# Kernel optimization log

Measured on AMD Instinct MI355X. Metric: run time of the kernel, lower is better.

The kernel has to match this reference:

```python
import jax, jax.numpy as jnp
import numpy as np

S, B, H, V = 64, 8, 512, 8192  # seq_length, batch, hidden, vocab
NEG = -1e9  # finite stand-in for -inf so gradients stay clean


def setup_inputs() -> dict:
    key = jax.random.key(0)
    ks = jax.random.split(key, 8)
    lin = lambda k, fi, fo: jax.random.normal(k, (fi, fo), jnp.float32) * 0.05
    return dict(
        h=jax.random.normal(ks[0], (S, B, H), jnp.float32) * 0.1,
        sentence=jax.random.randint(ks[1], (S, B), 0, V),
        t_W1=lin(ks[2], 2 * H, H), t_b1=jnp.zeros((H,), jnp.float32),
        t_W2=lin(ks[3], H, 1), t_b2=jnp.zeros((1,), jnp.float32),
        w_W1=lin(ks[4], 2 * H, H), w_b1=jnp.zeros((H,), jnp.float32),
        w_W2=lin(ks[5], H, V), w_b2=jnp.zeros((V,), jnp.float32),
    )


def _inside(h, sentence, t_W1, t_b1, t_W2, t_b2, w_W1, w_b1, w_W2, w_b2):
    sent_length = S - 1
    # ---- transition scores on full (i, j) grid: concat(h_i, h_j) -> MLP -> scalar
    hi = jnp.broadcast_to(h[:, None], (S, S, B, H))
    hj = jnp.broadcast_to(h[None, :], (S, S, B, H))
    feat = jnp.concatenate([hi, hj], axis=-1)                      # [S,S,B,2H]
    t = (jax.nn.relu(feat @ t_W1 + t_b1) @ t_W2 + t_b2)[..., 0]    # [S,S,B]
    sh_lp = jax.nn.log_sigmoid(-t)   # log p(shift | i, j)
    re_lp = jax.nn.log_sigmoid(t)    # log p(reduce | i, j)

    # ---- word generation log-probs for pairs (i, j), i < j <= sent_length-1
    iu, ju = jnp.triu_indices(sent_length, k=1)                    # P pairs
    hp = jnp.concatenate([h[iu], h[ju]], axis=-1)                  # [P,B,2H]
    logits = jax.nn.relu(hp @ w_W1 + w_b1) @ w_W2 + w_b2           # [P,B,V]
    lse = jax.scipy.special.logsumexp(logits, axis=-1)             # [P,B]
    tok = sentence[ju + 1]                                         # [P,B]
    tok_logit = jnp.take_along_axis(logits, tok[..., None], axis=-1)[..., 0]
    word_lp = tok_logit - lse
    # shift prob + word prob (word_prob_list in the original)
    wp = jnp.full((S, S, B), NEG, jnp.float32).at[iu, ju].set(sh_lp[iu, ju] + word_lp)

    # ---- DP table init
    table = jnp.full((S, S, B), NEG, jnp.float32)
    f0 = jnp.concatenate([h[0], h[0]], axis=-1)                    # [B,2H]
    lg0 = jax.nn.relu(f0 @ w_W1 + w_b1) @ w_W2 + w_b2              # [B,V]
    init_lp = jnp.take_along_axis(jax.nn.log_softmax(lg0, axis=-1),
                                  sentence[1][:, None], axis=1)[:, 0]
    table = table.at[0, 1].set(init_lp)
    jd = jnp.arange(1, sent_length)
    table = table.at[jd, jd + 1].set(0.0)

    # ---- diagonal sweep: table[i,j] = LSE_k( table[i,k]+table[k,j]+wp[i,k]+re[k,j] )
    ivec = jnp.arange(S)
    mvec = jnp.arange(1, S)

    def step(tab, g):
        i = ivec[:, None]
        m = mvec[None, :]
        k = jnp.clip(i + m, 0, S - 1)                              # [S,S-1]
        jv = jnp.clip(ivec + g, 0, S - 1)                          # [S]
        j = jv[:, None]
        valid = (m < g) & (ivec[:, None] + g <= sent_length)       # [S,S-1]
        sc = tab[i, k] + tab[k, j] + wp[i, k] + re_lp[k, j]        # [S,S-1,B]
        sc = jnp.where(valid[..., None], sc, NEG)
        mmax = jnp.max(sc, axis=1, keepdims=True)
        new = jnp.log(jnp.sum(jnp.exp(sc - mmax), axis=1)) + mmax[:, 0]
        row_ok = (ivec + g <= sent_length)[:, None]
        tab = tab.at[ivec, jv].set(jnp.where(row_ok, new, tab[ivec, jv]))
        return tab, None

    table, _ = jax.lax.scan(step, table, jnp.arange(2, sent_length + 1))
    final = table[0, sent_length] + re_lp[0, sent_length]          # [B]
    return -jnp.sum(final)  # neg_log_likelihood


def reference(h, sentence, t_W1, t_b1, t_W2, t_b2, w_W1, w_b1, w_W2, w_b2):
    return _inside(h, sentence, t_W1, t_b1, t_W2, t_b2, w_W1, w_b1, w_W2, w_b2)
```

## Files before the change

### kernel.cpp

```cpp
#include <hip/hip_runtime.h>
#include <hip/hip_bf16.h>
#include <hip/hip_fp8.h>
#include <math.h>

#define NEG (-1.0e9f)

typedef __bf16 bf16_t;
typedef __bf16 bf16x4 __attribute__((ext_vector_type(4)));
typedef __bf16 bf16x8 __attribute__((ext_vector_type(8)));
typedef float f32x4 __attribute__((ext_vector_type(4)));
typedef long i64x2 __attribute__((ext_vector_type(2)));
typedef unsigned char u8;
typedef unsigned long long u64;

#define SS 64
#define BB 8
#define HH 512
#define VV 8192
#define NPAIR 1953
#define NPTOT 1954
#define MROWS (NPTOT*BB)
#define MPAD  16384

__device__ __forceinline__ float logsig(float x) {
  return fminf(x, 0.f) - __logf(1.f + __expf(-fabsf(x)));
}
__device__ __forceinline__ u8 f2q(float x) { __hip_fp8_e4m3 q(x); return q.__x; }
__device__ __forceinline__ float q2f(u8 b) { __hip_fp8_e4m3 q; q.__x = b; return (float)q; }
__device__ __forceinline__ int ksl(int c) { return 2 * (c & 3) + (c >> 2); }

__global__ __launch_bounds__(256) void k_prep(
    const float* __restrict__ h,   bf16_t* __restrict__ hbf,
    const float* __restrict__ tW1, bf16_t* __restrict__ tW1T,
    const float* __restrict__ wW1, bf16_t* __restrict__ wW1T) {
  __shared__ float tile[32][33];
  int blk = blockIdx.x, tid = threadIdx.x;
  if (blk < 256) {
    int gi = blk * 256 + tid;
    float4 v = ((const float4*)h)[gi];
    bf16x4 o = {(bf16_t)v.x, (bf16_t)v.y, (bf16_t)v.z, (bf16_t)v.w};
    ((bf16x4*)hbf)[gi] = o;
    return;
  }
  const float* in; bf16_t* out; int R = 1024, C = 512, t;
  if (blk < 768) { in = tW1; out = tW1T; t = blk - 256; }
  else           { in = wW1; out = wW1T; t = blk - 768; }
  int xt = C / 32;
  int c0 = (t % xt) * 32, r0 = (t / xt) * 32;
  int tx = tid & 31, ty = tid >> 5;
  for (int i = ty; i < 32; i += 8)
    tile[i][tx] = in[(size_t)(r0 + i) * C + c0 + tx];
  __syncthreads();
  for (int i = ty; i < 32; i += 8)
    out[(size_t)(c0 + i) * R + r0 + tx] = (bf16_t)tile[tx][i];
}

__global__ __launch_bounds__(256) void k_gemm4t(
    const bf16_t* __restrict__ A,
    const bf16_t* __restrict__ tW1T, const bf16_t* __restrict__ wW1T,
    float* __restrict__ Ut, float* __restrict__ Vt,
    float* __restrict__ Uw, float* __restrict__ Vw,
    const float* __restrict__ wW2, u8* __restrict__ w2t8)
{
  __shared__ __align__(16) char lds_raw[16384];
  const int tid = threadIdx.x;
  if (blockIdx.x >= 64) {
    float* tile = (float*)lds_raw;
    int t = blockIdx.x - 64;
    int c0 = (t % 256) * 32, r0 = (t / 256) * 32;
    int tx = tid & 31, ty = tid >> 5;
    for (int i = ty; i < 32; i += 8)
      tile[i * 33 + tx] = wW2[(size_t)(r0 + i) * 8192 + c0 + tx];
    __syncthreads();
    for (int i = ty; i < 32; i += 8) {
      int k = r0 + tx;
      int pos = (k >> 6) * 64 + ksl((k >> 3) & 7) * 8 + (k & 7);
      w2t8[(size_t)(c0 + i) * 512 + pos] = f2q(tile[tx * 33 + i]);
    }
    return;
  }
  bf16_t* As = (bf16_t*)lds_raw;
  bf16_t* Bs = (bf16_t*)(lds_raw + 8192);
  const int lane = tid & 63;
  const int wave = tid >> 6;
  const int wr = wave >> 1, wc = wave & 1;
  const int sel = blockIdx.x >> 4, sub = blockIdx.x & 15;
  const bf16_t* BT = (sel < 2 ? tW1T : wW1T) + (sel & 1) * 512;
  float* Cout = (sel == 0) ? Ut : (sel == 1) ? Vt : (sel == 2) ? Uw : Vw;
  const int m0 = (sub & 3) * 128, n0 = (sub >> 2) * 128;
  const int lda = 512, ldb = 1024, ldc = 512;

  const int rowS = tid >> 2;
  const int kS = (tid & 3) * 8;
  const bf16_t* gA0 = A + (size_t)(m0 + rowS) * lda + kS;
  const bf16_t* gA1 = A + (size_t)(m0 + rowS + 64) * lda + kS;
  const bf16_t* gB0 = BT + (size_t)(n0 + rowS) * ldb + kS;
  const bf16_t* gB1 = BT + (size_t)(n0 + rowS + 64) * ldb + kS;

  f32x4 acc[4][4] = {};
  const int aoff = (wr * 64 + (lane & 15)) * 32 + (lane >> 4) * 8;
  const int boff = (wc * 64 + (lane & 15)) * 32 + (lane >> 4) * 8;

  for (int k0 = 0; k0 < 512; k0 += 32) {
    __builtin_amdgcn_global_load_lds((const __attribute__((address_space(1))) void*)(gA0 + k0),
        (__attribute__((address_space(3))) void*)(As + wave * 512), 16, 0, 0);
    __builtin_amdgcn_global_load_lds((const __attribute__((address_space(1))) void*)(gA1 + k0),
        (__attribute__((address_space(3))) void*)(As + 2048 + wave * 512), 16, 0, 0);
    __builtin_amdgcn_global_load_lds((const __attribute__((address_space(1))) void*)(gB0 + k0),
        (__attribute__((address_space(3))) void*)(Bs + wave * 512), 16, 0, 0);
    __builtin_amdgcn_global_load_lds((const __attribute__((address_space(1))) void*)(gB1 + k0),
        (__attribute__((address_space(3))) void*)(Bs + 2048 + wave * 512), 16, 0, 0);
    __syncthreads();
    bf16x8 af[4], bfr[4];
    #pragma unroll
    for (int mf = 0; mf < 4; ++mf) af[mf] = *(const bf16x8*)&As[aoff + mf * 16 * 32];
    #pragma unroll
    for (int nf = 0; nf < 4; ++nf) bfr[nf] = *(const bf16x8*)&Bs[boff + nf * 16 * 32];
    #pragma unroll
    for (int mf = 0; mf < 4; ++mf)
      #pragma unroll
      for (int nf = 0; nf < 4; ++nf)
        acc[mf][nf] = __builtin_amdgcn_mfma_f32_16x16x32_bf16(af[mf], bfr[nf], acc[mf][nf], 0, 0, 0);
    __syncthreads();
  }
  #pragma unroll
  for (int mf = 0; mf < 4; ++mf)
    #pragma unroll
    for (int r2 = 0; r2 < 4; ++r2) {
      int grow = m0 + wr * 64 + mf * 16 + (lane >> 4) * 4 + r2;
      #pragma unroll
      for (int nf = 0; nf < 4; ++nf) {
        int gcol = n0 + wc * 64 + nf * 16 + (lane & 15);
        Cout[(size_t)grow * ldc + gcol] = acc[mf][nf][r2];
      }
    }
}

#define STAGEA(b, h, kt) do { \
  const u8* _s = A8 + (size_t)(m0 + (h)*128 + (tid>>2)) * 512 + (kt)*64 + csrc; \
  __builtin_amdgcn_global_load_lds((const __attribute__((address_space(1))) void*)_s, \
    (__attribute__((address_space(3))) void*)(As + (b)*16384 + (h)*8192 + (tid>>6)*1024), 16, 0, 0); \
} while(0)

#define STAGEB(b, h, kt) do { \
  const u8* _s = BT8 + (size_t)(n0 + (h)*128 + (tid>>2)) * 512 + (kt)*64 + csrc; \
  __builtin_amdgcn_global_load_lds((const __attribute__((address_space(1))) void*)_s, \
    (__attribute__((address_space(3))) void*)(Bs + (b)*16384 + (h)*8192 + (tid>>6)*1024), 16, 0, 0); \
} while(0)

#define LDA(b, mh) do { \
  _Pragma("unroll") \
  for (int _m = 0; _m < 4; ++_m) \
    afv[_m] = *(const i64x2*)(As + (b)*16384 + (mh)*8192 + ardE + _m*1024); \
} while(0)

#define LDB(b, nh) do { \
  _Pragma("unroll") \
  for (int _n = 0; _n < 2; ++_n) \
    bfv[nh][_n] = *(const i64x2*)(Bs + (b)*16384 + (nh)*8192 + brdE + _n*1024); \
} while(0)

#define MMA(mh, nh) do { \
  __builtin_amdgcn_s_setprio(1); \
  _Pragma("unroll") \
  for (int _m = 0; _m < 4; ++_m) \
    _Pragma("unroll") \
    for (int _n = 0; _n < 2; ++_n) { \
      acc[(mh)*4+_m][(nh)*2+_n] = __builtin_amdgcn_mfma_f32_16x16x32_fp8_fp8( \
          afv[_m][0], bfv[nh][_n][0], acc[(mh)*4+_m][(nh)*2+_n], 0, 0, 0); \
      acc[(mh)*4+_m][(nh)*2+_n] = __builtin_amdgcn_mfma_f32_16x16x32_fp8_fp8( \
          afv[_m][1], bfv[nh][_n][1], acc[(mh)*4+_m][(nh)*2+_n], 0, 0, 0); \
    } \
  __builtin_amdgcn_s_setprio(0); \
} while(0)

#define BARLG() do { __builtin_amdgcn_s_barrier(); \
  asm volatile("s_waitcnt lgkmcnt(0)" ::: "memory"); \
  __builtin_amdgcn_sched_barrier(0); } while(0)
#define ENDPH() __builtin_amdgcn_s_barrier()
#define CKPT() asm volatile("s_waitcnt vmcnt(2)" ::: "memory")

__global__ __launch_bounds__(512, 2) void k_gemm256(
    const u8* __restrict__ A8,
    const u8* __restrict__ BT8,
    const float* __restrict__ bias,
    float* __restrict__ sumexp)
{
  __shared__ __align__(16) u8 As[2 * 16384];
  __shared__ __align__(16) u8 Bs[2 * 16384];
  const int tid = threadIdx.x;
  const int l = tid & 63;
  const int wave = tid >> 6;
  const int wr = wave >> 2, wc = wave & 3;

  const int xcd = blockIdx.x & 7, sub = blockIdx.x >> 3;
  const int mt = xcd * 8 + (sub & 7);
  const int nt = sub >> 3;
  const int m0 = mt * 256, n0 = nt * 256;

  const int csrc = (((tid & 3) ^ ((tid >> 3) & 3)) << 4);
  const int rsw = (((l >> 4) ^ ((l & 15) >> 1)) & 3) << 4;
  const int ardE = (wr * 64 + (l & 15)) * 64 + rsw;
  const int brdE = (wc * 32 + (l & 15)) * 64 + rsw;

  f32x4 acc[8][4] = {};
  i64x2 afv[4];
  i64x2 bfv[2][2];

  STAGEA(0, 0, 0); STAGEA(0, 1, 0); STAGEB(0, 0, 0); STAGEB(0, 1, 0);
  STAGEA(1, 0, 1); STAGEB(1, 0, 1);
  CKPT();
  __builtin_amdgcn_s_barrier();

  #pragma unroll 1
  for (int t = 0; t < 4; ++t) {
    int tA = 2 * t + 1;
    int tB = 2 * t + 2; if (tB > 7) tB = 7;
    int tC = 2 * t + 3; if (tC > 7) tC = 7;
    LDA(0, 0); LDB(0, 0); LDB(0, 1); STAGEA(1, 1, tA); STAGEB(1, 1, tA);
      BARLG(); MMA(0, 0); MMA(0, 1); ENDPH();
    LDA(0, 1);                       STAGEA(0, 0, tB); STAGEB(0, 0, tB);
      BARLG(); MMA(1, 0); MMA(1, 1); CKPT(); ENDPH();
    LDA(1, 0); LDB(1, 0); LDB(1, 1); STAGEA(0, 1, tB); STAGEB(0, 1, tB);
      BARLG(); MMA(0, 0); MMA(0, 1); ENDPH();
    LDA(1, 1);                       STAGEA(1, 0, tC); STAGEB(1, 0, tC);
      BARLG(); MMA(1, 0); MMA(1, 1); CKPT(); ENDPH();
  }

  float b2v[4];
  #pragma unroll
  for (int nf = 0; nf < 4; ++nf)
    b2v[nf] = bias[n0 + (nf >> 1) * 128 + wc * 32 + (nf & 1) * 16 + (l & 15)];
  #pragma unroll
  for (int mf = 0; mf < 8; ++mf) {
    #pragma unroll
    for (int r2 = 0; r2 < 4; ++r2) {
      float s = 0.f;
      #pragma unroll
      for (int nf = 0; nf < 4; ++nf)
        s += __expf(acc[mf][nf][r2] + b2v[nf]);
      s += __shfl_xor(s, 1); s += __shfl_xor(s, 2);
      s += __shfl_xor(s, 4); s += __shfl_xor(s, 8);
      if ((l & 15) == 0)
        atomicAdd(&sumexp[m0 + (mf >> 2) * 128 + wr * 64 + (mf & 3) * 16 + (l >> 4) * 4 + r2], s);
    }
  }
}

__global__ __launch_bounds__(256) void k_actnet(
    const float* __restrict__ Uw, const float* __restrict__ Vw,
    const float* __restrict__ wb1, u8* __restrict__ act8,
    float* __restrict__ sumexp,
    const u8* __restrict__ w2t8, const int* __restrict__ sent,
    const float* __restrict__ wb2, float* __restrict__ tok_logit,
    const float* __restrict__ Ut, const float* __restrict__ Vt,
    const float* __restrict__ tb1, const float* __restrict__ tW2,
    const float* __restrict__ tb2,
    float* __restrict__ sh_lp, float* __restrict__ re_lp)
{
  __shared__ float ldsf[8192];
  if (blockIdx.x < 2048) {
    float* pd = ldsf;
    int p = blockIdx.x;
    if (threadIdx.x < 8) sumexp[p * 8 + threadIdx.x] = 0.f;
    int iu = 0, ju = 0;
    bool real = (p < NPTOT);
    if (p < NPAIR) {
      int i = 0, base = 0;
      while (base + (62 - i) <= p) { base += 62 - i; ++i; }
      iu = i; ju = i + 1 + (p - base);
    }
    const int srow = (p < NPAIR) ? (ju + 1) : 1;
    for (int t = threadIdx.x; t < 512; t += 256) {
      int b = t >> 6, c = t & 63;
      int wpos = (c >> 3) * 64 + ksl(c & 7) * 8;
      u64 bytes = 0;
      if (real) {
        const float4* u4 = (const float4*)(Uw + (size_t)(iu * BB + b) * HH);
        const float4* v4 = (const float4*)(Vw + (size_t)(ju * BB + b) * HH);
        const float4* bb4 = (const float4*)wb1;
        #pragma unroll
        for (int q = 0; q < 2; ++q) {
          float4 uu = u4[c * 2 + q], vv = v4[c * 2 + q], bb = bb4[c * 2 + q];
          bytes |= (u64)f2q(fmaxf(uu.x + vv.x + bb.x, 0.f)) << (8 * (q * 4 + 0));
          bytes |= (u64)f2q(fmaxf(uu.y + vv.y + bb.y, 0.f)) << (8 * (q * 4 + 1));
          bytes |= (u64)f2q(fmaxf(uu.z + vv.z + bb.z, 0.f)) << (8 * (q * 4 + 2));
          bytes |= (u64)f2q(fmaxf(uu.w + vv.w + bb.w, 0.f)) << (8 * (q * 4 + 3));
        }
      }
      *(u64*)(act8 + (size_t)(p * 8 + b) * 512 + wpos) = bytes;
      float s = 0.f;
      if (real) {
        int tok = sent[srow * BB + b];
        u64 wv = *(const u64*)(w2t8 + (size_t)tok * 512 + wpos);
        #pragma unroll
        for (int e = 0; e < 8; ++e)
          s += q2f((u8)(bytes >> (8 * e))) * q2f((u8)(wv >> (8 * e)));
      }
      pd[t] = s;
    }
    __syncthreads();
    if (real) {
      int wv_ = threadIdx.x >> 6, ln = threadIdx.x & 63;
      #pragma unroll
      for (int rr = 0; rr < 2; ++rr) {
        int b = wv_ * 2 + rr;
        float s = pd[b * 64 + ln];
        #pragma unroll
        for (int off = 1; off < 64; off <<= 1) s += __shfl_xor(s, off);
        if (ln == 0) {
          int tok = sent[srow * BB + b];
          tok_logit[p * 8 + b] = s + wb2[tok];
        }
      }
    }
    return;
  }
  int t = blockIdx.x - 2048;
  int b = t & 7, pr = t >> 3;
  int ig = 0, base = 0;
  while (base + (8 - ig) <= pr) { base += 8 - ig; ++ig; }
  int jg = ig + (pr - base);
  float* Us = ldsf;
  float* Vs = ldsf + 4096;
  for (int q = threadIdx.x; q < 1024; q += 256) {
    int ii = q >> 7, cc = q & 127;
    ((float4*)Us)[ii * 128 + cc] = ((const float4*)(Ut + (size_t)((ig * 8 + ii) * BB + b) * HH))[cc];
    ((float4*)Vs)[ii * 128 + cc] = ((const float4*)(Vt + (size_t)((jg * 8 + ii) * BB + b) * HH))[cc];
  }
  __syncthreads();
  int lane = threadIdx.x & 63, wv_ = threadIdx.x >> 6;
  float b1r[8], w2r[8];
  #pragma unroll
  for (int k = 0; k < 8; ++k) { b1r[k] = tb1[lane + 64 * k]; w2r[k] = tW2[lane + 64 * k]; }
  for (int pp = wv_; pp < 64; pp += 4) {
    int ii = pp >> 3, jj = pp & 7;
    int i = ig * 8 + ii, j = jg * 8 + jj;
    float s = 0.f;
    #pragma unroll
    for (int k = 0; k < 8; ++k)
      s += fmaxf(Us[ii * 512 + lane + 64 * k] + Vs[jj * 512 + lane + 64 * k] + b1r[k], 0.f) * w2r[k];
    #pragma unroll
    for (int off = 1; off < 64; off <<= 1) s += __shfl_xor(s, off);
    if (lane == 0 && i < j) {
      float tv = s + tb2[0];
      re_lp[(i * 64 + j) * 8 + b] = logsig(tv);
      sh_lp[(i * 64 + j) * 8 + b] = logsig(-tv);
    }
  }
}

__global__ __launch_bounds__(1024) void k_dp(const float* __restrict__ sh_lp, const float* __restrict__ re_lp,
                                             const float* __restrict__ tok_logit, const float* __restrict__ sumexp,
                                             float* __restrict__ finals) {
  int b = blockIdx.x;
  __shared__ float tab[4096];
  __shared__ float wpl[4096];
  __shared__ float rel[4096];
  int tid = threadIdx.x;
  for (int idx = tid; idx < 4096; idx += 1024) {
    tab[idx] = NEG;
    int i = idx >> 6, j = idx & 63;
    float w = NEG;
    if (i < j && j <= 62) {
      int p = i * 62 - i * (i - 1) / 2 + (j - i - 1);
      int r = p * 8 + b;
      w = sh_lp[idx * 8 + b] + (tok_logit[r] - __logf(sumexp[r]));
    }
    wpl[idx] = w;
    rel[idx] = (idx >> 6) < (idx & 63) ? re_lp[idx * 8 + b] : NEG;
  }
  __syncthreads();
  if (tid == 0) tab[1] = tok_logit[NPAIR * 8 + b] - __logf(sumexp[NPAIR * 8 + b]);
  if (tid >= 1 && tid <= 62) tab[tid * 64 + tid + 1] = 0.f;
  __syncthreads();
  int lane = tid & 63, wave = tid >> 6;
  for (int g = 2; g <= 63; ++g) {
    int cnt = 64 - g;
    if (g <= 17) {
      int seg = lane >> 4, sl = lane & 15;
      int i = wave * 4 + seg;
      if (i < cnt) {
        int m = sl + 1;
        int j = i + g, k = i + m;
        float sc = NEG;
        if (m < g) sc = tab[i * 64 + k] + tab[k * 64 + j] + wpl[i * 64 + k] + rel[k * 64 + j];
        float mx = sc;
        #pragma unroll
        for (int off = 1; off < 16; off <<= 1) mx = fmaxf(mx, __shfl_xor(mx, off));
        float e = (m < g) ? __expf(sc - mx) : 0.f;
        #pragma unroll
        for (int off = 1; off < 16; off <<= 1) e += __shfl_xor(e, off);
        if (sl == 0) tab[i * 64 + j] = __logf(e) + mx;
      }
    } else {
      for (int i = wave; i < cnt; i += 16) {
        int m = lane + 1;
        int j = i + g, k = i + m;
        float sc = NEG;
        if (m < g) sc = tab[i * 64 + k] + tab[k * 64 + j] + wpl[i * 64 + k] + rel[k * 64 + j];
        float mx = sc;
        #pragma unroll
        for (int off = 1; off < 64; off <<= 1) mx = fmaxf(mx, __shfl_xor(mx, off));
        float e = (m < g) ? __expf(sc - mx) : 0.f;
        #pragma unroll
        for (int off = 1; off < 64; off <<= 1) e += __shfl_xor(e, off);
        if (lane == 0) tab[i * 64 + j] = __logf(e) + mx;
      }
    }
    __syncthreads();
  }
  if (tid == 0) finals[b] = tab[63] + rel[63];
}

__global__ void k_final(const float* __restrict__ finals, float* __restrict__ out) {
  if (threadIdx.x == 0) {
    float s = 0.f;
    for (int b = 0; b < 8; ++b) s += finals[b];
    out[0] = -s;
  }
}

extern "C" void kernel_launch(void* const* d_in, const int* in_sizes, int n_in,
                              void* d_out, int out_size, void* d_ws, size_t ws_size,
                              hipStream_t stream) {
  const float* h    = (const float*)d_in[0];
  const int*   sent = (const int*)d_in[1];
  const float* tW1  = (const float*)d_in[2];
  const float* tb1  = (const float*)d_in[3];
  const float* tW2  = (const float*)d_in[4];
  const float* tb2  = (const float*)d_in[5];
  const float* wW1  = (const float*)d_in[6];
  const float* wb1  = (const float*)d_in[7];
  const float* wW2  = (const float*)d_in[8];
  const float* wb2  = (const float*)d_in[9];
  float* out = (float*)d_out;

  char* ws = (char*)d_ws;
  size_t off = 0;
  auto alloc = [&](size_t bytes) { char* p = ws + off; off += (bytes + 255) & ~(size_t)255; return p; };
  bf16_t* hbf    = (bf16_t*)alloc((size_t)512 * 512 * 2);
  bf16_t* tW1T   = (bf16_t*)alloc((size_t)512 * 1024 * 2);
  bf16_t* wW1T   = (bf16_t*)alloc((size_t)512 * 1024 * 2);
  u8*     w2t8   = (u8*)alloc((size_t)VV * HH);
  float*  Ut     = (float*)alloc((size_t)512 * 512 * 4);
  float*  Vt     = (float*)alloc((size_t)512 * 512 * 4);
  float*  Uw     = (float*)alloc((size_t)512 * 512 * 4);
  float*  Vw     = (float*)alloc((size_t)512 * 512 * 4);
  u8*     act8   = (u8*)alloc((size_t)MPAD * HH);
  float*  sumexp = (float*)alloc((size_t)MPAD * 4);
  float*  tokl   = (float*)alloc((size_t)MPAD * 4);
  float*  shlp   = (float*)alloc((size_t)32768 * 4);
  float*  relp   = (float*)alloc((size_t)32768 * 4);
  float*  finals = (float*)alloc(256);

  k_prep<<<1280, 256, 0, stream>>>(h, hbf, tW1, tW1T, wW1, wW1T);
  k_gemm4t<<<4160, 256, 0, stream>>>(hbf, tW1T, wW1T, Ut, Vt, Uw, Vw, wW2, w2t8);
  k_actnet<<<2048 + 288, 256, 0, stream>>>(Uw, Vw, wb1, act8, sumexp, w2t8, sent, wb2, tokl,
                                           Ut, Vt, tb1, tW2, tb2, shlp, relp);
  k_gemm256<<<2048, 512, 0, stream>>>(act8, w2t8, wb2, sumexp);
  k_dp<<<8, 1024, 0, stream>>>(shlp, relp, tokl, sumexp, finals);
  k_final<<<1, 64, 0, stream>>>(finals, out);
}
```

Before: 288.9 us.

## Deepen GEMM LDS pipeline to four stages and pre-fold DP table terms

The fp8 GEMM kernel moves from a two-buffer, barrier-per-phase schedule to a four-stage LDS ring. It now uses one barrier per two k-tiles, issues bulk global->LDS prefetches, and double-buffers the A fragments with partial lgkmcnt waits. This is meant to cut barrier and wait stalls, but occupancy drops from 2 blocks per CU to 1 because LDS use doubles. The DP kernel stores the table pre-added with the word and reduce log-probs, with the reduce side transposed, so each score needs two contiguous LDS reads instead of four scattered ones.

```diff
diff --git a/kernel.cpp b/kernel.cpp
--- a/kernel.cpp
+++ b/kernel.cpp
@@ -136,58 +136,57 @@
     }
 }
 
-#define STAGEA(b, h, kt) do { \
+#define STAGEA(s, h, kt) do { \
   const u8* _s = A8 + (size_t)(m0 + (h)*128 + (tid>>2)) * 512 + (kt)*64 + csrc; \
   __builtin_amdgcn_global_load_lds((const __attribute__((address_space(1))) void*)_s, \
-    (__attribute__((address_space(3))) void*)(As + (b)*16384 + (h)*8192 + (tid>>6)*1024), 16, 0, 0); \
+    (__attribute__((address_space(3))) void*)(As + (s)*16384 + (h)*8192 + (tid>>6)*1024), 16, 0, 0); \
 } while(0)
 
-#define STAGEB(b, h, kt) do { \
+#define STAGEB(s, h, kt) do { \
   const u8* _s = BT8 + (size_t)(n0 + (h)*128 + (tid>>2)) * 512 + (kt)*64 + csrc; \
   __builtin_amdgcn_global_load_lds((const __attribute__((address_space(1))) void*)_s, \
-    (__attribute__((address_space(3))) void*)(Bs + (b)*16384 + (h)*8192 + (tid>>6)*1024), 16, 0, 0); \
+    (__attribute__((address_space(3))) void*)(Bs + (s)*16384 + (h)*8192 + (tid>>6)*1024), 16, 0, 0); \
 } while(0)
 
-#define LDA(b, mh) do { \
+#define LDAx(s, mh, dst) do { \
   _Pragma("unroll") \
   for (int _m = 0; _m < 4; ++_m) \
-    afv[_m] = *(const i64x2*)(As + (b)*16384 + (mh)*8192 + ardE + _m*1024); \
+    dst[_m] = *(const i64x2*)(As + (s)*16384 + (mh)*8192 + ardE + _m*1024); \
 } while(0)
 
-#define LDB(b, nh) do { \
+#define LDB(s, nh) do { \
   _Pragma("unroll") \
   for (int _n = 0; _n < 2; ++_n) \
-    bfv[nh][_n] = *(const i64x2*)(Bs + (b)*16384 + (nh)*8192 + brdE + _n*1024); \
+    bfv[nh][_n] = *(const i64x2*)(Bs + (s)*16384 + (nh)*8192 + brdE + _n*1024); \
 } while(0)
 
-#define MMA(mh, nh) do { \
+#define MMA(AF, mh, nh) do { \
   __builtin_amdgcn_s_setprio(1); \
   _Pragma("unroll") \
   for (int _m = 0; _m < 4; ++_m) \
     _Pragma("unroll") \
     for (int _n = 0; _n < 2; ++_n) { \
       acc[(mh)*4+_m][(nh)*2+_n] = __builtin_amdgcn_mfma_f32_16x16x32_fp8_fp8( \
-          afv[_m][0], bfv[nh][_n][0], acc[(mh)*4+_m][(nh)*2+_n], 0, 0, 0); \
+          AF[_m][0], bfv[nh][_n][0], acc[(mh)*4+_m][(nh)*2+_n], 0, 0, 0); \
       acc[(mh)*4+_m][(nh)*2+_n] = __builtin_amdgcn_mfma_f32_16x16x32_fp8_fp8( \
-          afv[_m][1], bfv[nh][_n][1], acc[(mh)*4+_m][(nh)*2+_n], 0, 0, 0); \
+          AF[_m][1], bfv[nh][_n][1], acc[(mh)*4+_m][(nh)*2+_n], 0, 0, 0); \
     } \
   __builtin_amdgcn_s_setprio(0); \
 } while(0)
 
-#define BARLG() do { __builtin_amdgcn_s_barrier(); \
-  asm volatile("s_waitcnt lgkmcnt(0)" ::: "memory"); \
+#define WAIT_LGKM(n) do { \
+  asm volatile("s_waitcnt lgkmcnt(" #n ")" ::: "memory"); \
   __builtin_amdgcn_sched_barrier(0); } while(0)
-#define ENDPH() __builtin_amdgcn_s_barrier()
-#define CKPT() asm volatile("s_waitcnt vmcnt(2)" ::: "memory")
-
-__global__ __launch_bounds__(512, 2) void k_gemm256(
+#define WAIT_VM0() asm volatile("s_waitcnt vmcnt(0)" ::: "memory")
+
+__global__ __launch_bounds__(512, 1) void k_gemm256(
     const u8* __restrict__ A8,
     const u8* __restrict__ BT8,
     const float* __restrict__ bias,
     float* __restrict__ sumexp)
 {
-  __shared__ __align__(16) u8 As[2 * 16384];
-  __shared__ __align__(16) u8 Bs[2 * 16384];
+  __shared__ __align__(16) u8 As[4 * 16384];
+  __shared__ __align__(16) u8 Bs[4 * 16384];
   const int tid = threadIdx.x;
   const int l = tid & 63;
   const int wave = tid >> 6;
@@ -204,27 +203,33 @@
   const int brdE = (wc * 32 + (l & 15)) * 64 + rsw;
 
   f32x4 acc[8][4] = {};
-  i64x2 afv[4];
+  i64x2 afv0[4], afv1[4];
   i64x2 bfv[2][2];
 
   STAGEA(0, 0, 0); STAGEA(0, 1, 0); STAGEB(0, 0, 0); STAGEB(0, 1, 0);
-  STAGEA(1, 0, 1); STAGEB(1, 0, 1);
-  CKPT();
-  __builtin_amdgcn_s_barrier();
+  STAGEA(1, 0, 1); STAGEA(1, 1, 1); STAGEB(1, 0, 1); STAGEB(1, 1, 1);
 
   #pragma unroll 1
-  for (int t = 0; t < 4; ++t) {
-    int tA = 2 * t + 1;
-    int tB = 2 * t + 2; if (tB > 7) tB = 7;
-    int tC = 2 * t + 3; if (tC > 7) tC = 7;
-    LDA(0, 0); LDB(0, 0); LDB(0, 1); STAGEA(1, 1, tA); STAGEB(1, 1, tA);
-      BARLG(); MMA(0, 0); MMA(0, 1); ENDPH();
-    LDA(0, 1);                       STAGEA(0, 0, tB); STAGEB(0, 0, tB);
-      BARLG(); MMA(1, 0); MMA(1, 1); CKPT(); ENDPH();
-    LDA(1, 0); LDB(1, 0); LDB(1, 1); STAGEA(0, 1, tB); STAGEB(0, 1, tB);
-      BARLG(); MMA(0, 0); MMA(0, 1); ENDPH();
-    LDA(1, 1);                       STAGEA(1, 0, tC); STAGEB(1, 0, tC);
-      BARLG(); MMA(1, 0); MMA(1, 1); CKPT(); ENDPH();
+  for (int u = 0; u < 4; ++u) {
+    const int sa = (u & 1) * 2, sb = sa + 1;
+    const int ssA = ((u + 1) & 1) * 2, ssB = ssA + 1;
+    int tA = 2 * u + 2; if (tA > 7) tA = 7;
+    int tB = 2 * u + 3; if (tB > 7) tB = 7;
+
+    WAIT_VM0();
+    __builtin_amdgcn_s_barrier();
+
+    STAGEA(ssA, 0, tA); STAGEA(ssA, 1, tA); STAGEB(ssA, 0, tA); STAGEB(ssA, 1, tA);
+    STAGEB(ssB, 0, tB); STAGEB(ssB, 1, tB); STAGEA(ssB, 0, tB); STAGEA(ssB, 1, tB);
+
+    LDAx(sa, 0, afv0); LDB(sa, 0); LDB(sa, 1);
+    LDAx(sa, 1, afv1);
+    WAIT_LGKM(4);  MMA(afv0, 0, 0); MMA(afv0, 0, 1);
+    WAIT_LGKM(0);  MMA(afv1, 1, 0); MMA(afv1, 1, 1);
+    LDAx(sb, 0, afv0); LDB(sb, 0); LDB(sb, 1);
+    LDAx(sb, 1, afv1);
+    WAIT_LGKM(4);  MMA(afv0, 0, 0); MMA(afv0, 0, 1);
+    WAIT_LGKM(0);  MMA(afv1, 1, 0); MMA(afv1, 1, 1);
   }
 
   float b2v[4];
@@ -354,12 +359,12 @@
                                              const float* __restrict__ tok_logit, const float* __restrict__ sumexp,
                                              float* __restrict__ finals) {
   int b = blockIdx.x;
-  __shared__ float tab[4096];
-  __shared__ float wpl[4096];
-  __shared__ float rel[4096];
+  __shared__ float tw[4096];
+  __shared__ float trT[4096];
+  __shared__ float wplL[4096];
+  __shared__ float relL[4096];
   int tid = threadIdx.x;
   for (int idx = tid; idx < 4096; idx += 1024) {
-    tab[idx] = NEG;
     int i = idx >> 6, j = idx & 63;
     float w = NEG;
     if (i < j && j <= 62) {
@@ -367,12 +372,24 @@
       int r = p * 8 + b;
       w = sh_lp[idx * 8 + b] + (tok_logit[r] - __logf(sumexp[r]));
     }
-    wpl[idx] = w;
-    rel[idx] = (idx >> 6) < (idx & 63) ? re_lp[idx * 8 + b] : NEG;
+    wplL[idx] = w;
+    relL[idx] = (i < j) ? re_lp[idx * 8 + b] : NEG;
   }
   __syncthreads();
-  if (tid == 0) tab[1] = tok_logit[NPAIR * 8 + b] - __logf(sumexp[NPAIR * 8 + b]);
-  if (tid >= 1 && tid <= 62) tab[tid * 64 + tid + 1] = 0.f;
+  for (int idx = tid; idx < 4096; idx += 1024) {
+    tw[idx] = NEG + wplL[idx];
+    trT[idx] = NEG + relL[(idx & 63) * 64 + (idx >> 6)];
+  }
+  __syncthreads();
+  if (tid == 0) {
+    float v0 = tok_logit[NPAIR * 8 + b] - __logf(sumexp[NPAIR * 8 + b]);
+    tw[1] = v0 + wplL[1];
+    trT[1 * 64 + 0] = v0 + relL[0 * 64 + 1];
+  }
+  if (tid >= 1 && tid <= 62) {
+    tw[tid * 64 + tid + 1] = wplL[tid * 64 + tid + 1];
+    trT[(tid + 1) * 64 + tid] = relL[tid * 64 + tid + 1];
+  }
   __syncthreads();
   int lane = tid & 63, wave = tid >> 6;
   for (int g = 2; g <= 63; ++g) {
@@ -383,34 +400,40 @@
       if (i < cnt) {
         int m = sl + 1;
         int j = i + g, k = i + m;
-        float sc = NEG;
-        if (m < g) sc = tab[i * 64 + k] + tab[k * 64 + j] + wpl[i * 64 + k] + rel[k * 64 + j];
+        float sc = (m < g) ? tw[i * 64 + k] + trT[j * 64 + k] : NEG;
         float mx = sc;
         #pragma unroll
         for (int off = 1; off < 16; off <<= 1) mx = fmaxf(mx, __shfl_xor(mx, off));
         float e = (m < g) ? __expf(sc - mx) : 0.f;
         #pragma unroll
         for (int off = 1; off < 16; off <<= 1) e += __shfl_xor(e, off);
-        if (sl == 0) tab[i * 64 + j] = __logf(e) + mx;
+        if (sl == 0) {
+          float val = __logf(e) + mx;
+          tw[i * 64 + j] = val + wplL[i * 64 + j];
+          trT[j * 64 + i] = val + relL[i * 64 + j];
+        }
       }
     } else {
       for (int i = wave; i < cnt; i += 16) {
         int m = lane + 1;
         int j = i + g, k = i + m;
-        float sc = NEG;
-        if (m < g) sc = tab[i * 64 + k] + tab[k * 64 + j] + wpl[i * 64 + k] + rel[k * 64 + j];
+        float sc = (m < g) ? tw[i * 64 + k] + trT[j * 64 + k] : NEG;
         float mx = sc;
         #pragma unroll
         for (int off = 1; off < 64; off <<= 1) mx = fmaxf(mx, __shfl_xor(mx, off));
         float e = (m < g) ? __expf(sc - mx) : 0.f;
         #pragma unroll
         for (int off = 1; off < 64; off <<= 1) e += __shfl_xor(e, off);
-        if (lane == 0) tab[i * 64 + j] = __logf(e) + mx;
+        if (lane == 0) {
+          float val = __logf(e) + mx;
+          tw[i * 64 + j] = val + wplL[i * 64 + j];
+          trT[j * 64 + i] = val + relL[i * 64 + j];
+        }
       }
     }
     __syncthreads();
   }
-  if (tid == 0) finals[b] = tab[63] + rel[63];
+  if (tid == 0) finals[b] = trT[63 * 64 + 0];
 }
 
 __global__ void k_final(const float* __restrict__ finals, float* __restrict__ out) {
```

Result: faster. 267.1 us (-7.5%).

## Replace sumexp atomics with partial sums, prefold DP terms, pack fp8 conversions

Applied to the files above, without the earlier changes.

The GEMM epilogue no longer does global atomicAdds. It reduces each block's row sums in LDS and writes one per-column-tile partial sum, which the DP kernel then adds up over 32 slices. The DP kernel keeps the table with wp and re already folded in and stores the re-side in transposed form, so each inner step reads two LDS values with unit stride instead of four. The actnet kernel uses packed fp8 convert intrinsics in place of per-byte conversions. The trade-off is extra reads of the partials in the DP kernel's setup, plus an added barrier and LDS reuse in the GEMM epilogue.

```diff
diff --git a/kernel.cpp b/kernel.cpp
--- a/kernel.cpp
+++ b/kernel.cpp
@@ -8,9 +8,11 @@
 typedef __bf16 bf16_t;
 typedef __bf16 bf16x4 __attribute__((ext_vector_type(4)));
 typedef __bf16 bf16x8 __attribute__((ext_vector_type(8)));
+typedef float f32x2 __attribute__((ext_vector_type(2)));
 typedef float f32x4 __attribute__((ext_vector_type(4)));
 typedef long i64x2 __attribute__((ext_vector_type(2)));
 typedef unsigned char u8;
+typedef unsigned int u32;
 typedef unsigned long long u64;
 
 #define SS 64
@@ -26,7 +28,6 @@
   return fminf(x, 0.f) - __logf(1.f + __expf(-fabsf(x)));
 }
 __device__ __forceinline__ u8 f2q(float x) { __hip_fp8_e4m3 q(x); return q.__x; }
-__device__ __forceinline__ float q2f(u8 b) { __hip_fp8_e4m3 q; q.__x = b; return (float)q; }
 __device__ __forceinline__ int ksl(int c) { return 2 * (c & 3) + (c >> 2); }
 
 __global__ __launch_bounds__(256) void k_prep(
@@ -184,7 +185,7 @@
     const u8* __restrict__ A8,
     const u8* __restrict__ BT8,
     const float* __restrict__ bias,
-    float* __restrict__ sumexp)
+    float* __restrict__ psum)
 {
   __shared__ __align__(16) u8 As[2 * 16384];
   __shared__ __align__(16) u8 Bs[2 * 16384];
@@ -227,10 +228,12 @@
       BARLG(); MMA(1, 0); MMA(1, 1); CKPT(); ENDPH();
   }
 
+  __syncthreads();
   float b2v[4];
   #pragma unroll
   for (int nf = 0; nf < 4; ++nf)
     b2v[nf] = bias[n0 + (nf >> 1) * 128 + wc * 32 + (nf & 1) * 16 + (l & 15)];
+  float* eL = (float*)As;
   #pragma unroll
   for (int mf = 0; mf < 8; ++mf) {
     #pragma unroll
@@ -242,15 +245,19 @@
       s += __shfl_xor(s, 1); s += __shfl_xor(s, 2);
       s += __shfl_xor(s, 4); s += __shfl_xor(s, 8);
       if ((l & 15) == 0)
-        atomicAdd(&sumexp[m0 + (mf >> 2) * 128 + wr * 64 + (mf & 3) * 16 + (l >> 4) * 4 + r2], s);
-    }
+        eL[wc * 256 + (mf >> 2) * 128 + wr * 64 + (mf & 3) * 16 + (l >> 4) * 4 + r2] = s;
+    }
+  }
+  __syncthreads();
+  if (tid < 256) {
+    float v = eL[tid] + eL[256 + tid] + eL[512 + tid] + eL[768 + tid];
+    psum[(size_t)nt * MPAD + m0 + tid] = v;
   }
 }
 
 __global__ __launch_bounds__(256) void k_actnet(
     const float* __restrict__ Uw, const float* __restrict__ Vw,
     const float* __restrict__ wb1, u8* __restrict__ act8,
-    float* __restrict__ sumexp,
     const u8* __restrict__ w2t8, const int* __restrict__ sent,
     const float* __restrict__ wb2, float* __restrict__ tok_logit,
     const float* __restrict__ Ut, const float* __restrict__ Vt,
@@ -262,7 +269,6 @@
   if (blockIdx.x < 2048) {
     float* pd = ldsf;
     int p = blockIdx.x;
-    if (threadIdx.x < 8) sumexp[p * 8 + threadIdx.x] = 0.f;
     int iu = 0, ju = 0;
     bool real = (p < NPTOT);
     if (p < NPAIR) {
@@ -275,28 +281,37 @@
       int b = t >> 6, c = t & 63;
       int wpos = (c >> 3) * 64 + ksl(c & 7) * 8;
       u64 bytes = 0;
+      float s = 0.f;
       if (real) {
         const float4* u4 = (const float4*)(Uw + (size_t)(iu * BB + b) * HH);
         const float4* v4 = (const float4*)(Vw + (size_t)(ju * BB + b) * HH);
         const float4* bb4 = (const float4*)wb1;
+        int dw[2] = {0, 0};
         #pragma unroll
         for (int q = 0; q < 2; ++q) {
           float4 uu = u4[c * 2 + q], vv = v4[c * 2 + q], bb = bb4[c * 2 + q];
-          bytes |= (u64)f2q(fmaxf(uu.x + vv.x + bb.x, 0.f)) << (8 * (q * 4 + 0));
-          bytes |= (u64)f2q(fmaxf(uu.y + vv.y + bb.y, 0.f)) << (8 * (q * 4 + 1));
-          bytes |= (u64)f2q(fmaxf(uu.z + vv.z + bb.z, 0.f)) << (8 * (q * 4 + 2));
-          bytes |= (u64)f2q(fmaxf(uu.w + vv.w + bb.w, 0.f)) << (8 * (q * 4 + 3));
+          float v0 = fmaxf(uu.x + vv.x + bb.x, 0.f);
+          float v1 = fmaxf(uu.y + vv.y + bb.y, 0.f);
+          float v2 = fmaxf(uu.z + vv.z + bb.z, 0.f);
+          float v3 = fmaxf(uu.w + vv.w + bb.w, 0.f);
+          dw[q] = __builtin_amdgcn_cvt_pk_fp8_f32(v0, v1, dw[q], false);
+          dw[q] = __builtin_amdgcn_cvt_pk_fp8_f32(v2, v3, dw[q], true);
+        }
+        bytes = (u64)(u32)dw[0] | ((u64)(u32)dw[1] << 32);
+        int tok = sent[srow * BB + b];
+        u64 wv = *(const u64*)(w2t8 + (size_t)tok * 512 + wpos);
+        int aw[2] = {(int)(u32)bytes, (int)(u32)(bytes >> 32)};
+        int ww[2] = {(int)(u32)wv, (int)(u32)(wv >> 32)};
+        #pragma unroll
+        for (int q = 0; q < 2; ++q) {
+          f32x2 alo = __builtin_amdgcn_cvt_pk_f32_fp8(aw[q], false);
+          f32x2 ahi = __builtin_amdgcn_cvt_pk_f32_fp8(aw[q], true);
+          f32x2 wlo = __builtin_amdgcn_cvt_pk_f32_fp8(ww[q], false);
+          f32x2 whi = __builtin_amdgcn_cvt_pk_f32_fp8(ww[q], true);
+          s += alo[0] * wlo[0] + alo[1] * wlo[1] + ahi[0] * whi[0] + ahi[1] * whi[1];
         }
       }
       *(u64*)(act8 + (size_t)(p * 8 + b) * 512 + wpos) = bytes;
-      float s = 0.f;
-      if (real) {
-        int tok = sent[srow * BB + b];
-        u64 wv = *(const u64*)(w2t8 + (size_t)tok * 512 + wpos);
-        #pragma unroll
-        for (int e = 0; e < 8; ++e)
-          s += q2f((u8)(bytes >> (8 * e))) * q2f((u8)(wv >> (8 * e)));
-      }
       pd[t] = s;
     }
     __syncthreads();
@@ -351,28 +366,47 @@
 }
 
 __global__ __launch_bounds__(1024) void k_dp(const float* __restrict__ sh_lp, const float* __restrict__ re_lp,
-                                             const float* __restrict__ tok_logit, const float* __restrict__ sumexp,
+                                             const float* __restrict__ tok_logit, const float* __restrict__ psum,
                                              float* __restrict__ finals) {
   int b = blockIdx.x;
-  __shared__ float tab[4096];
-  __shared__ float wpl[4096];
-  __shared__ float rel[4096];
+  __shared__ float tw[4096];
+  __shared__ float trT[4096];
+  __shared__ float wplL[4096];
+  __shared__ float relL[4096];
   int tid = threadIdx.x;
   for (int idx = tid; idx < 4096; idx += 1024) {
-    tab[idx] = NEG;
     int i = idx >> 6, j = idx & 63;
     float w = NEG;
     if (i < j && j <= 62) {
       int p = i * 62 - i * (i - 1) / 2 + (j - i - 1);
       int r = p * 8 + b;
-      w = sh_lp[idx * 8 + b] + (tok_logit[r] - __logf(sumexp[r]));
-    }
-    wpl[idx] = w;
-    rel[idx] = (idx >> 6) < (idx & 63) ? re_lp[idx * 8 + b] : NEG;
-  }
-  __syncthreads();
-  if (tid == 0) tab[1] = tok_logit[NPAIR * 8 + b] - __logf(sumexp[NPAIR * 8 + b]);
-  if (tid >= 1 && tid <= 62) tab[tid * 64 + tid + 1] = 0.f;
+      float se = 0.f;
+      #pragma unroll 8
+      for (int sl2 = 0; sl2 < 32; ++sl2) se += psum[(size_t)sl2 * MPAD + r];
+      w = sh_lp[idx * 8 + b] + (tok_logit[r] - __logf(se));
+    }
+    wplL[idx] = w;
+    relL[idx] = (i < j) ? re_lp[idx * 8 + b] : NEG;
+  }
+  __syncthreads();
+  for (int idx = tid; idx < 4096; idx += 1024) {
+    tw[idx] = NEG + wplL[idx];
+    trT[idx] = NEG + relL[(idx & 63) * 64 + (idx >> 6)];
+  }
+  __syncthreads();
+  if (tid == 0) {
+    int r0i = NPAIR * 8 + b;
+    float se = 0.f;
+    #pragma unroll 8
+    for (int sl2 = 0; sl2 < 32; ++sl2) se += psum[(size_t)sl2 * MPAD + r0i];
+    float v0 = tok_logit[r0i] - __logf(se);
+    tw[1] = v0 + wplL[1];
+    trT[1 * 64 + 0] = v0 + relL[0 * 64 + 1];
+  }
+  if (tid >= 1 && tid <= 62) {
+    tw[tid * 64 + tid + 1] = wplL[tid * 64 + tid + 1];
+    trT[(tid + 1) * 64 + tid] = relL[tid * 64 + tid + 1];
+  }
   __syncthreads();
   int lane = tid & 63, wave = tid >> 6;
   for (int g = 2; g <= 63; ++g) {
@@ -383,34 +417,40 @@
       if (i < cnt) {
         int m = sl + 1;
         int j = i + g, k = i + m;
-        float sc = NEG;
-        if (m < g) sc = tab[i * 64 + k] + tab[k * 64 + j] + wpl[i * 64 + k] + rel[k * 64 + j];
+        float sc = (m < g) ? tw[i * 64 + k] + trT[j * 64 + k] : NEG;
         float mx = sc;
         #pragma unroll
         for (int off = 1; off < 16; off <<= 1) mx = fmaxf(mx, __shfl_xor(mx, off));
         float e = (m < g) ? __expf(sc - mx) : 0.f;
         #pragma unroll
         for (int off = 1; off < 16; off <<= 1) e += __shfl_xor(e, off);
-        if (sl == 0) tab[i * 64 + j] = __logf(e) + mx;
+        if (sl == 0) {
+          float val = __logf(e) + mx;
+          tw[i * 64 + j] = val + wplL[i * 64 + j];
+          trT[j * 64 + i] = val + relL[i * 64 + j];
+        }
       }
     } else {
       for (int i = wave; i < cnt; i += 16) {
         int m = lane + 1;
         int j = i + g, k = i + m;
-        float sc = NEG;
-        if (m < g) sc = tab[i * 64 + k] + tab[k * 64 + j] + wpl[i * 64 + k] + rel[k * 64 + j];
+        float sc = (m < g) ? tw[i * 64 + k] + trT[j * 64 + k] : NEG;
         float mx = sc;
         #pragma unroll
         for (int off = 1; off < 64; off <<= 1) mx = fmaxf(mx, __shfl_xor(mx, off));
         float e = (m < g) ? __expf(sc - mx) : 0.f;
         #pragma unroll
         for (int off = 1; off < 64; off <<= 1) e += __shfl_xor(e, off);
-        if (lane == 0) tab[i * 64 + j] = __logf(e) + mx;
+        if (lane == 0) {
+          float val = __logf(e) + mx;
+          tw[i * 64 + j] = val + wplL[i * 64 + j];
+          trT[j * 64 + i] = val + relL[i * 64 + j];
+        }
       }
     }
     __syncthreads();
   }
-  if (tid == 0) finals[b] = tab[63] + rel[63];
+  if (tid == 0) finals[b] = trT[63 * 64 + 0];
 }
 
 __global__ void k_final(const float* __restrict__ finals, float* __restrict__ out) {
@@ -448,7 +488,7 @@
   float*  Uw     = (float*)alloc((size_t)512 * 512 * 4);
   float*  Vw     = (float*)alloc((size_t)512 * 512 * 4);
   u8*     act8   = (u8*)alloc((size_t)MPAD * HH);
-  float*  sumexp = (float*)alloc((size_t)MPAD * 4);
+  float*  psum   = (float*)alloc((size_t)32 * MPAD * 4);
   float*  tokl   = (float*)alloc((size_t)MPAD * 4);
   float*  shlp   = (float*)alloc((size_t)32768 * 4);
   float*  relp   = (float*)alloc((size_t)32768 * 4);
@@ -456,9 +496,9 @@
 
   k_prep<<<1280, 256, 0, stream>>>(h, hbf, tW1, tW1T, wW1, wW1T);
   k_gemm4t<<<4160, 256, 0, stream>>>(hbf, tW1T, wW1T, Ut, Vt, Uw, Vw, wW2, w2t8);
-  k_actnet<<<2048 + 288, 256, 0, stream>>>(Uw, Vw, wb1, act8, sumexp, w2t8, sent, wb2, tokl,
+  k_actnet<<<2048 + 288, 256, 0, stream>>>(Uw, Vw, wb1, act8, w2t8, sent, wb2, tokl,
                                            Ut, Vt, tb1, tW2, tb2, shlp, relp);
-  k_gemm256<<<2048, 512, 0, stream>>>(act8, w2t8, wb2, sumexp);
-  k_dp<<<8, 1024, 0, stream>>>(shlp, relp, tokl, sumexp, finals);
+  k_gemm256<<<2048, 512, 0, stream>>>(act8, w2t8, wb2, psum);
+  k_dp<<<8, 1024, 0, stream>>>(shlp, relp, tokl, psum, finals);
   k_final<<<1, 64, 0, stream>>>(finals, out);
 }
```

Measured after the change: 292.4 us. No clear change (+1.2%).
